# Kernel optimization log

Measured on AMD Instinct MI355X. Metric: run time of the kernel, lower is better.

Reference implementation:

```python
import jax, jax.numpy as jnp
import numpy as np

TOP_K = 2


def setup_inputs() -> dict:
    key = jax.random.key(0)
    k1, k2, k3, k4, k5 = jax.random.split(key, 5)
    T, H, I, E = 1024, 1024, 2816, 8
    return {
        "hidden_states": jax.random.normal(k1, (T, H), dtype=jnp.float32),
        "router_logits": jax.random.normal(k2, (T, E), dtype=jnp.float32),
        "w1": jax.random.normal(k3, (E, I, H), dtype=jnp.float32) * 0.02,
        "w3": jax.random.normal(k4, (E, I, H), dtype=jnp.float32) * 0.02,
        "w2": jax.random.normal(k5, (E, H, I), dtype=jnp.float32) * 0.02,
    }


def _gate_weights(router_logits):
    # top-k softmax with renormalization (Mixtral-style routing)
    probs = jax.nn.softmax(router_logits, axis=-1)          # [T, E]
    vals, idx = jax.lax.top_k(probs, TOP_K)                  # [T, K]
    vals = vals / jnp.sum(vals, axis=-1, keepdims=True)
    E = router_logits.shape[-1]
    # dense per-expert gate [T, E]: scatter top-k weights via one-hot
    onehot = jax.nn.one_hot(idx, E, dtype=vals.dtype)        # [T, K, E]
    return jnp.einsum("tk,tke->te", vals, onehot)


def reference(hidden_states, router_logits, w1, w3, w2):
    x = hidden_states.reshape(-1, hidden_states.shape[-1])   # [T, H]
    gate = _gate_weights(router_logits)                      # [T, E]
    # GatedMLP per expert: silu(x @ w1^T) * (x @ w3^T) @ w2^T
    h1 = jnp.einsum("th,eih->tei", x, w1)                    # [T, E, I]
    h3 = jnp.einsum("th,eih->tei", x, w3)
    act = jax.nn.silu(h1) * h3                               # [T, E, I]
    y = jnp.einsum("tei,ehi->teh", act, w2)                  # [T, E, H]
    out = jnp.einsum("teh,te->th", y, gate)                  # weighted combine
    return out
```

## Files before the change

### kernel.cpp

```cpp
#include <hip/hip_runtime.h>
#include <stdint.h>

#define T_TOK 1024
#define H_DIM 1024
#define I_DIM 2816
#define E_NUM 8
#define KSPLIT 4
#define K2_STEPS (I_DIM / 64 / KSPLIT)

typedef __attribute__((ext_vector_type(8))) short bf16x8;
typedef __attribute__((ext_vector_type(4))) float f32x4;

struct Meta { int counts[E_NUM]; int tiles[E_NUM]; int offs[E_NUM]; };

__device__ __forceinline__ unsigned short f2b(float f) {
    unsigned u = __float_as_uint(f);
    u += 0x7fffu + ((u >> 16) & 1u);
    return (unsigned short)(u >> 16);
}

__device__ __forceinline__ uint4 pack8(const float4 a, const float4 b) {
    union { unsigned short us[8]; uint4 v; } u;
    u.us[0] = f2b(a.x); u.us[1] = f2b(a.y); u.us[2] = f2b(a.z); u.us[3] = f2b(a.w);
    u.us[4] = f2b(b.x); u.us[5] = f2b(b.y); u.us[6] = f2b(b.z); u.us[7] = f2b(b.w);
    return u.v;
}

__global__ void route_kernel(const float* __restrict__ logits,
                             int* __restrict__ tok, float* __restrict__ gate,
                             Meta* __restrict__ meta) {
    __shared__ int cnt[E_NUM];
    const int tid = threadIdx.x;
    if (tid < E_NUM) cnt[tid] = 0;
    for (int j = tid; j < E_NUM * T_TOK; j += 1024) { tok[j] = 0; gate[j] = 0.f; }
    __syncthreads();

    float p[E_NUM];
    const float* lrow = logits + tid * E_NUM;
    float m = -1e30f;
    #pragma unroll
    for (int e = 0; e < E_NUM; ++e) { p[e] = lrow[e]; m = fmaxf(m, p[e]); }
    #pragma unroll
    for (int e = 0; e < E_NUM; ++e) p[e] = __expf(p[e] - m);
    int e0 = 0; float v0 = p[0];
    #pragma unroll
    for (int e = 1; e < E_NUM; ++e) if (p[e] > v0) { v0 = p[e]; e0 = e; }
    int e1 = -1; float v1 = -1.f;
    #pragma unroll
    for (int e = 0; e < E_NUM; ++e) if (e != e0 && p[e] > v1) { v1 = p[e]; e1 = e; }
    const float inv = 1.f / (v0 + v1);
    const float g0 = v0 * inv, g1 = v1 * inv;

    const int p0 = atomicAdd(&cnt[e0], 1);
    const int p1 = atomicAdd(&cnt[e1], 1);
    tok[e0 * T_TOK + p0] = tid; gate[e0 * T_TOK + p0] = g0;
    tok[e1 * T_TOK + p1] = tid; gate[e1 * T_TOK + p1] = g1;
    __syncthreads();
    if (tid == 0) {
        int off = 0;
        for (int e = 0; e < E_NUM; ++e) {
            const int c = cnt[e];
            const int t = (c + 127) >> 7;
            meta->counts[e] = c; meta->tiles[e] = t; meta->offs[e] = off;
            off += t * 128;
        }
    }
}

__global__ void cvt_x_kernel(const float* __restrict__ x, unsigned short* __restrict__ xb) {
    const int i = blockIdx.x * blockDim.x + threadIdx.x;
    const float4 v = ((const float4*)x)[i];
    ushort4 o; o.x = f2b(v.x); o.y = f2b(v.y); o.z = f2b(v.z); o.w = f2b(v.w);
    ((ushort4*)xb)[i] = o;
}

__launch_bounds__(512)
__global__ void gemm1_kernel(const unsigned short* __restrict__ xb,
                             const float* __restrict__ w1,
                             const float* __restrict__ w3,
                             const int* __restrict__ tok,
                             const Meta* __restrict__ meta,
                             unsigned short* __restrict__ act) {
    const int e = blockIdx.y;
    const int mt = blockIdx.z;
    if (mt >= meta->tiles[e]) return;
    const int it = blockIdx.x;
    const int tid = threadIdx.x;

    __shared__ __align__(16) unsigned short As[128 * 64];
    __shared__ __align__(16) unsigned short B1s[64 * 64];
    __shared__ __align__(16) unsigned short B3s[64 * 64];

    const int srow = tid >> 3, ssub = tid & 7;
    const int t0 = tok[e * T_TOK + mt * 128 + srow];
    const int t1 = tok[e * T_TOK + mt * 128 + 64 + srow];
    const unsigned short* ap0 = xb + (size_t)t0 * H_DIM + ssub * 8;
    const unsigned short* ap1 = xb + (size_t)t1 * H_DIM + ssub * 8;
    const int scol = (ssub * 8) ^ ((srow & 7) << 3);
    unsigned short* al0 = &As[srow * 64 + scol];
    unsigned short* al1 = &As[(64 + srow) * 64 + scol];

    const size_t wbase = (size_t)e * I_DIM * H_DIM + (size_t)(it * 64 + srow) * H_DIM + ssub * 8;
    const float* b1p = w1 + wbase;
    const float* b3p = w3 + wbase;
    unsigned short* bl1 = &B1s[srow * 64 + scol];
    unsigned short* bl3 = &B3s[srow * 64 + scol];

    const int wave = tid >> 6, lane = tid & 63;
    const int quad = lane >> 4, l15 = lane & 15;
    const int mbase = (wave >> 1) * 32;
    const int nbase = (wave & 1) * 32;

    f32x4 acc1[2][2], acc3[2][2];
    #pragma unroll
    for (int m = 0; m < 2; ++m)
        #pragma unroll
        for (int n = 0; n < 2; ++n) {
            acc1[m][n] = (f32x4){0.f, 0.f, 0.f, 0.f};
            acc3[m][n] = (f32x4){0.f, 0.f, 0.f, 0.f};
        }

    uint4 ra0 = *(const uint4*)ap0, ra1 = *(const uint4*)ap1;
    float4 rb1a = *(const float4*)b1p, rb1b = *(const float4*)(b1p + 4);
    float4 rb3a = *(const float4*)b3p, rb3b = *(const float4*)(b3p + 4);

    const int NK = H_DIM / 64;
    for (int ks = 0; ks < NK; ++ks) {
        __syncthreads();
        *(uint4*)al0 = ra0;
        *(uint4*)al1 = ra1;
        *(uint4*)bl1 = pack8(rb1a, rb1b);
        *(uint4*)bl3 = pack8(rb3a, rb3b);
        __syncthreads();
        if (ks + 1 < NK) {
            const int k0 = (ks + 1) * 64;
            ra0 = *(const uint4*)(ap0 + k0);  ra1 = *(const uint4*)(ap1 + k0);
            rb1a = *(const float4*)(b1p + k0); rb1b = *(const float4*)(b1p + k0 + 4);
            rb3a = *(const float4*)(b3p + k0); rb3b = *(const float4*)(b3p + k0 + 4);
        }
        bf16x8 a[2][2], bf1[2][2], bf3[2][2];
        #pragma unroll
        for (int m = 0; m < 2; ++m) {
            const int row = mbase + m * 16 + l15;
            #pragma unroll
            for (int kk = 0; kk < 2; ++kk)
                a[m][kk] = *(const bf16x8*)&As[row * 64 + ((kk * 32 + quad * 8) ^ ((row & 7) << 3))];
        }
        #pragma unroll
        for (int n = 0; n < 2; ++n) {
            const int row = nbase + n * 16 + l15;
            #pragma unroll
            for (int kk = 0; kk < 2; ++kk) {
                const int off = row * 64 + ((kk * 32 + quad * 8) ^ ((row & 7) << 3));
                bf1[n][kk] = *(const bf16x8*)&B1s[off];
                bf3[n][kk] = *(const bf16x8*)&B3s[off];
            }
        }
        #pragma unroll
        for (int m = 0; m < 2; ++m)
            #pragma unroll
            for (int n = 0; n < 2; ++n)
                #pragma unroll
                for (int kk = 0; kk < 2; ++kk) {
                    acc1[m][n] = __builtin_amdgcn_mfma_f32_16x16x32_bf16(a[m][kk], bf1[n][kk], acc1[m][n], 0, 0, 0);
                    acc3[m][n] = __builtin_amdgcn_mfma_f32_16x16x32_bf16(a[m][kk], bf3[n][kk], acc3[m][n], 0, 0, 0);
                }
    }

    const int opad = meta->offs[e];
    #pragma unroll
    for (int m = 0; m < 2; ++m)
        #pragma unroll
        for (int n = 0; n < 2; ++n)
            #pragma unroll
            for (int rr = 0; rr < 4; ++rr) {
                const float v1 = acc1[m][n][rr];
                const float v3 = acc3[m][n][rr];
                const float s = v1 / (1.f + __expf(-v1)) * v3;
                const int row = opad + mt * 128 + mbase + m * 16 + quad * 4 + rr;
                const int col = it * 64 + nbase + n * 16 + l15;
                act[(size_t)row * I_DIM + col] = f2b(s);
            }
}

__launch_bounds__(512)
__global__ void gemm2_kernel(const unsigned short* __restrict__ act,
                             const float* __restrict__ w2,
                             const int* __restrict__ tok,
                             const float* __restrict__ gate,
                             const Meta* __restrict__ meta,
                             float* __restrict__ out) {
    const int e = blockIdx.y;
    const int mt = blockIdx.z >> 2;
    const int kb = blockIdx.z & 3;
    if (mt >= meta->tiles[e]) return;
    const int it = blockIdx.x;
    const int tid = threadIdx.x;
    const int opad = meta->offs[e];

    __shared__ __align__(16) unsigned short As[128 * 64];
    __shared__ __align__(16) unsigned short Bs[64 * 64];

    const int srow = tid >> 3, ssub = tid & 7;
    const int kbase = kb * (K2_STEPS * 64);
    const unsigned short* ap0 = act + (size_t)(opad + mt * 128 + srow) * I_DIM + kbase + ssub * 8;
    const unsigned short* ap1 = ap0 + (size_t)64 * I_DIM;
    const int scol = (ssub * 8) ^ ((srow & 7) << 3);
    unsigned short* al0 = &As[srow * 64 + scol];
    unsigned short* al1 = &As[(64 + srow) * 64 + scol];

    const float* bp = w2 + (size_t)e * H_DIM * I_DIM + (size_t)(it * 64 + srow) * I_DIM + kbase + ssub * 8;
    unsigned short* bl = &Bs[srow * 64 + scol];

    const int wave = tid >> 6, lane = tid & 63;
    const int quad = lane >> 4, l15 = lane & 15;
    const int mbase = (wave >> 1) * 32;
    const int nbase = (wave & 1) * 32;

    f32x4 acc[2][2];
    #pragma unroll
    for (int m = 0; m < 2; ++m)
        #pragma unroll
        for (int n = 0; n < 2; ++n) acc[m][n] = (f32x4){0.f, 0.f, 0.f, 0.f};

    uint4 ra0 = *(const uint4*)ap0, ra1 = *(const uint4*)ap1;
    float4 rba = *(const float4*)bp, rbb = *(const float4*)(bp + 4);

    for (int ks = 0; ks < K2_STEPS; ++ks) {
        __syncthreads();
        *(uint4*)al0 = ra0;
        *(uint4*)al1 = ra1;
        *(uint4*)bl = pack8(rba, rbb);
        __syncthreads();
        if (ks + 1 < K2_STEPS) {
            const int k0 = (ks + 1) * 64;
            ra0 = *(const uint4*)(ap0 + k0); ra1 = *(const uint4*)(ap1 + k0);
            rba = *(const float4*)(bp + k0); rbb = *(const float4*)(bp + k0 + 4);
        }
        bf16x8 a[2][2], bf[2][2];
        #pragma unroll
        for (int m = 0; m < 2; ++m) {
            const int row = mbase + m * 16 + l15;
            #pragma unroll
            for (int kk = 0; kk < 2; ++kk)
                a[m][kk] = *(const bf16x8*)&As[row * 64 + ((kk * 32 + quad * 8) ^ ((row & 7) << 3))];
        }
        #pragma unroll
        for (int n = 0; n < 2; ++n) {
            const int row = nbase + n * 16 + l15;
            #pragma unroll
            for (int kk = 0; kk < 2; ++kk)
                bf[n][kk] = *(const bf16x8*)&Bs[row * 64 + ((kk * 32 + quad * 8) ^ ((row & 7) << 3))];
        }
        #pragma unroll
        for (int m = 0; m < 2; ++m)
            #pragma unroll
            for (int n = 0; n < 2; ++n)
                #pragma unroll
                for (int kk = 0; kk < 2; ++kk)
                    acc[m][n] = __builtin_amdgcn_mfma_f32_16x16x32_bf16(a[m][kk], bf[n][kk], acc[m][n], 0, 0, 0);
    }

    #pragma unroll
    for (int m = 0; m < 2; ++m)
        #pragma unroll
        for (int rr = 0; rr < 4; ++rr) {
            const int r = mt * 128 + mbase + m * 16 + quad * 4 + rr;
            const int t = tok[e * T_TOK + r];
            const float g = gate[e * T_TOK + r];
            if (g != 0.f) {
                #pragma unroll
                for (int n = 0; n < 2; ++n) {
                    const int col = it * 64 + nbase + n * 16 + l15;
                    atomicAdd(&out[(size_t)t * H_DIM + col], g * acc[m][n][rr]);
                }
            }
        }
}

extern "C" void kernel_launch(void* const* d_in, const int* in_sizes, int n_in,
                              void* d_out, int out_size, void* d_ws, size_t ws_size,
                              hipStream_t stream) {
    const float* x      = (const float*)d_in[0];
    const float* logits = (const float*)d_in[1];
    const float* w1     = (const float*)d_in[2];
    const float* w3     = (const float*)d_in[3];
    const float* w2     = (const float*)d_in[4];
    float* out = (float*)d_out;

    char* ws = (char*)d_ws;
    int*   tok  = (int*)ws;
    float* gate = (float*)(ws + 32768);
    Meta*  meta = (Meta*)(ws + 65536);
    unsigned short* xb  = (unsigned short*)(ws + 131072);
    unsigned short* act = (unsigned short*)(ws + 131072 + 2097152);

    hipMemsetAsync(d_out, 0, (size_t)T_TOK * H_DIM * sizeof(float), stream);
    route_kernel<<<1, 1024, 0, stream>>>(logits, tok, gate, meta);
    cvt_x_kernel<<<T_TOK * H_DIM / 4 / 256, 256, 0, stream>>>(x, xb);
    gemm1_kernel<<<dim3(I_DIM / 64, E_NUM, 8), 512, 0, stream>>>(xb, w1, w3, tok, meta, act);
    gemm2_kernel<<<dim3(H_DIM / 64, E_NUM, 8 * KSPLIT), 512, 0, stream>>>(act, w2, tok, gate, meta, out);
}
```

Baseline: 339.2 us.

## Double-buffer GEMM LDS tiles and replace atomic scatter with deterministic combine kernel

Both expert GEMMs now use two LDS buffers with register prefetch two steps ahead, so each iteration needs one barrier instead of two. The second GEMM drops from four K-splits to two and writes partial sums to a workspace instead of atomically adding into the output. A new combine kernel applies the gate weights and sums the two expert rows per token, which also removes the output memset. The cost is an extra launch and extra workspace traffic, and the doubled LDS use with occupancy hints may affect register allocation.

```diff
diff --git a/kernel.cpp b/kernel.cpp
--- a/kernel.cpp
+++ b/kernel.cpp
@@ -5,8 +5,9 @@
 #define H_DIM 1024
 #define I_DIM 2816
 #define E_NUM 8
-#define KSPLIT 4
+#define KSPLIT 2
 #define K2_STEPS (I_DIM / 64 / KSPLIT)
+#define MAXROWS 3072
 
 typedef __attribute__((ext_vector_type(8))) short bf16x8;
 typedef __attribute__((ext_vector_type(4))) float f32x4;
@@ -26,13 +27,17 @@
     return u.v;
 }
 
+#define SYNC_RAW() do { asm volatile("s_waitcnt lgkmcnt(0)" ::: "memory"); __builtin_amdgcn_s_barrier(); } while (0)
+
 __global__ void route_kernel(const float* __restrict__ logits,
-                             int* __restrict__ tok, float* __restrict__ gate,
+                             int* __restrict__ tok,
+                             int4* __restrict__ comb,
                              Meta* __restrict__ meta) {
     __shared__ int cnt[E_NUM];
+    __shared__ int soffs[E_NUM];
     const int tid = threadIdx.x;
     if (tid < E_NUM) cnt[tid] = 0;
-    for (int j = tid; j < E_NUM * T_TOK; j += 1024) { tok[j] = 0; gate[j] = 0.f; }
+    for (int j = tid; j < E_NUM * T_TOK; j += 1024) tok[j] = 0;
     __syncthreads();
 
     float p[E_NUM];
@@ -53,8 +58,8 @@
 
     const int p0 = atomicAdd(&cnt[e0], 1);
     const int p1 = atomicAdd(&cnt[e1], 1);
-    tok[e0 * T_TOK + p0] = tid; gate[e0 * T_TOK + p0] = g0;
-    tok[e1 * T_TOK + p1] = tid; gate[e1 * T_TOK + p1] = g1;
+    tok[e0 * T_TOK + p0] = tid;
+    tok[e1 * T_TOK + p1] = tid;
     __syncthreads();
     if (tid == 0) {
         int off = 0;
@@ -62,9 +67,13 @@
             const int c = cnt[e];
             const int t = (c + 127) >> 7;
             meta->counts[e] = c; meta->tiles[e] = t; meta->offs[e] = off;
+            soffs[e] = off;
             off += t * 128;
         }
     }
+    __syncthreads();
+    comb[tid] = make_int4(soffs[e0] + p0, soffs[e1] + p1,
+                          __float_as_int(g0), __float_as_int(g1));
 }
 
 __global__ void cvt_x_kernel(const float* __restrict__ x, unsigned short* __restrict__ xb) {
@@ -74,7 +83,7 @@
     ((ushort4*)xb)[i] = o;
 }
 
-__launch_bounds__(512)
+__launch_bounds__(512, 4)
 __global__ void gemm1_kernel(const unsigned short* __restrict__ xb,
                              const float* __restrict__ w1,
                              const float* __restrict__ w3,
@@ -87,9 +96,9 @@
     const int it = blockIdx.x;
     const int tid = threadIdx.x;
 
-    __shared__ __align__(16) unsigned short As[128 * 64];
-    __shared__ __align__(16) unsigned short B1s[64 * 64];
-    __shared__ __align__(16) unsigned short B3s[64 * 64];
+    __shared__ __align__(16) unsigned short As[2][128 * 64];
+    __shared__ __align__(16) unsigned short B1s[2][64 * 64];
+    __shared__ __align__(16) unsigned short B3s[2][64 * 64];
 
     const int srow = tid >> 3, ssub = tid & 7;
     const int t0 = tok[e * T_TOK + mt * 128 + srow];
@@ -97,14 +106,13 @@
     const unsigned short* ap0 = xb + (size_t)t0 * H_DIM + ssub * 8;
     const unsigned short* ap1 = xb + (size_t)t1 * H_DIM + ssub * 8;
     const int scol = (ssub * 8) ^ ((srow & 7) << 3);
-    unsigned short* al0 = &As[srow * 64 + scol];
-    unsigned short* al1 = &As[(64 + srow) * 64 + scol];
+    const int aoff0 = srow * 64 + scol;
+    const int aoff1 = (64 + srow) * 64 + scol;
+    const int boff  = srow * 64 + scol;
 
     const size_t wbase = (size_t)e * I_DIM * H_DIM + (size_t)(it * 64 + srow) * H_DIM + ssub * 8;
     const float* b1p = w1 + wbase;
     const float* b3p = w3 + wbase;
-    unsigned short* bl1 = &B1s[srow * 64 + scol];
-    unsigned short* bl3 = &B3s[srow * 64 + scol];
 
     const int wave = tid >> 6, lane = tid & 63;
     const int quad = lane >> 4, l15 = lane & 15;
@@ -120,52 +128,71 @@
             acc3[m][n] = (f32x4){0.f, 0.f, 0.f, 0.f};
         }
 
-    uint4 ra0 = *(const uint4*)ap0, ra1 = *(const uint4*)ap1;
-    float4 rb1a = *(const float4*)b1p, rb1b = *(const float4*)(b1p + 4);
-    float4 rb3a = *(const float4*)b3p, rb3b = *(const float4*)(b3p + 4);
+#define G1_LOAD(S, koff) do { \
+        S##_a0  = *(const uint4*)(ap0 + (koff));      S##_a1  = *(const uint4*)(ap1 + (koff)); \
+        S##_b1a = *(const float4*)(b1p + (koff));     S##_b1b = *(const float4*)(b1p + (koff) + 4); \
+        S##_b3a = *(const float4*)(b3p + (koff));     S##_b3b = *(const float4*)(b3p + (koff) + 4); \
+    } while (0)
+
+#define G1_STORE(S, B) do { \
+        *(uint4*)&As[B][aoff0] = S##_a0; \
+        *(uint4*)&As[B][aoff1] = S##_a1; \
+        *(uint4*)&B1s[B][boff] = pack8(S##_b1a, S##_b1b); \
+        *(uint4*)&B3s[B][boff] = pack8(S##_b3a, S##_b3b); \
+    } while (0)
+
+#define G1_COMPUTE(B) do { \
+        bf16x8 afr[2][2], f1[2][2], f3[2][2]; \
+        _Pragma("unroll") \
+        for (int m = 0; m < 2; ++m) { \
+            const int row = mbase + m * 16 + l15; \
+            _Pragma("unroll") \
+            for (int kk = 0; kk < 2; ++kk) \
+                afr[m][kk] = *(const bf16x8*)&As[B][row * 64 + ((kk * 32 + quad * 8) ^ ((row & 7) << 3))]; \
+        } \
+        _Pragma("unroll") \
+        for (int n = 0; n < 2; ++n) { \
+            const int row = nbase + n * 16 + l15; \
+            _Pragma("unroll") \
+            for (int kk = 0; kk < 2; ++kk) { \
+                const int off = row * 64 + ((kk * 32 + quad * 8) ^ ((row & 7) << 3)); \
+                f1[n][kk] = *(const bf16x8*)&B1s[B][off]; \
+                f3[n][kk] = *(const bf16x8*)&B3s[B][off]; \
+            } \
+        } \
+        _Pragma("unroll") \
+        for (int m = 0; m < 2; ++m) \
+            _Pragma("unroll") \
+            for (int n = 0; n < 2; ++n) \
+                _Pragma("unroll") \
+                for (int kk = 0; kk < 2; ++kk) { \
+                    acc1[m][n] = __builtin_amdgcn_mfma_f32_16x16x32_bf16(afr[m][kk], f1[n][kk], acc1[m][n], 0, 0, 0); \
+                    acc3[m][n] = __builtin_amdgcn_mfma_f32_16x16x32_bf16(afr[m][kk], f3[n][kk], acc3[m][n], 0, 0, 0); \
+                } \
+    } while (0)
+
+    uint4 s0_a0, s0_a1; float4 s0_b1a, s0_b1b, s0_b3a, s0_b3b;
+    uint4 s1_a0, s1_a1; float4 s1_b1a, s1_b1b, s1_b3a, s1_b3b;
 
     const int NK = H_DIM / 64;
-    for (int ks = 0; ks < NK; ++ks) {
-        __syncthreads();
-        *(uint4*)al0 = ra0;
-        *(uint4*)al1 = ra1;
-        *(uint4*)bl1 = pack8(rb1a, rb1b);
-        *(uint4*)bl3 = pack8(rb3a, rb3b);
-        __syncthreads();
-        if (ks + 1 < NK) {
-            const int k0 = (ks + 1) * 64;
-            ra0 = *(const uint4*)(ap0 + k0);  ra1 = *(const uint4*)(ap1 + k0);
-            rb1a = *(const float4*)(b1p + k0); rb1b = *(const float4*)(b1p + k0 + 4);
-            rb3a = *(const float4*)(b3p + k0); rb3b = *(const float4*)(b3p + k0 + 4);
-        }
-        bf16x8 a[2][2], bf1[2][2], bf3[2][2];
-        #pragma unroll
-        for (int m = 0; m < 2; ++m) {
-            const int row = mbase + m * 16 + l15;
-            #pragma unroll
-            for (int kk = 0; kk < 2; ++kk)
-                a[m][kk] = *(const bf16x8*)&As[row * 64 + ((kk * 32 + quad * 8) ^ ((row & 7) << 3))];
-        }
-        #pragma unroll
-        for (int n = 0; n < 2; ++n) {
-            const int row = nbase + n * 16 + l15;
-            #pragma unroll
-            for (int kk = 0; kk < 2; ++kk) {
-                const int off = row * 64 + ((kk * 32 + quad * 8) ^ ((row & 7) << 3));
-                bf1[n][kk] = *(const bf16x8*)&B1s[off];
-                bf3[n][kk] = *(const bf16x8*)&B3s[off];
-            }
-        }
-        #pragma unroll
-        for (int m = 0; m < 2; ++m)
-            #pragma unroll
-            for (int n = 0; n < 2; ++n)
-                #pragma unroll
-                for (int kk = 0; kk < 2; ++kk) {
-                    acc1[m][n] = __builtin_amdgcn_mfma_f32_16x16x32_bf16(a[m][kk], bf1[n][kk], acc1[m][n], 0, 0, 0);
-                    acc3[m][n] = __builtin_amdgcn_mfma_f32_16x16x32_bf16(a[m][kk], bf3[n][kk], acc3[m][n], 0, 0, 0);
-                }
+    G1_LOAD(s0, 0);
+    G1_STORE(s0, 0);
+    G1_LOAD(s1, 64);
+    SYNC_RAW();
+
+    for (int ks = 0; ks < NK; ks += 2) {
+        { const int k2 = (ks + 2 < NK) ? (ks + 2) * 64 : 0; G1_LOAD(s0, k2); }
+        G1_COMPUTE(0);
+        G1_STORE(s1, 1);
+        SYNC_RAW();
+        { const int k3 = (ks + 3 < NK) ? (ks + 3) * 64 : 0; G1_LOAD(s1, k3); }
+        G1_COMPUTE(1);
+        G1_STORE(s0, 0);
+        SYNC_RAW();
     }
+#undef G1_LOAD
+#undef G1_STORE
+#undef G1_COMPUTE
 
     const int opad = meta->offs[e];
     #pragma unroll
@@ -183,34 +210,32 @@
             }
 }
 
-__launch_bounds__(512)
+__launch_bounds__(512, 4)
 __global__ void gemm2_kernel(const unsigned short* __restrict__ act,
                              const float* __restrict__ w2,
-                             const int* __restrict__ tok,
-                             const float* __restrict__ gate,
                              const Meta* __restrict__ meta,
-                             float* __restrict__ out) {
+                             float* __restrict__ ybuf) {
     const int e = blockIdx.y;
-    const int mt = blockIdx.z >> 2;
-    const int kb = blockIdx.z & 3;
+    const int mt = blockIdx.z >> 1;
+    const int kb = blockIdx.z & 1;
     if (mt >= meta->tiles[e]) return;
     const int it = blockIdx.x;
     const int tid = threadIdx.x;
     const int opad = meta->offs[e];
 
-    __shared__ __align__(16) unsigned short As[128 * 64];
-    __shared__ __align__(16) unsigned short Bs[64 * 64];
+    __shared__ __align__(16) unsigned short As[2][128 * 64];
+    __shared__ __align__(16) unsigned short Bs[2][64 * 64];
 
     const int srow = tid >> 3, ssub = tid & 7;
     const int kbase = kb * (K2_STEPS * 64);
     const unsigned short* ap0 = act + (size_t)(opad + mt * 128 + srow) * I_DIM + kbase + ssub * 8;
     const unsigned short* ap1 = ap0 + (size_t)64 * I_DIM;
     const int scol = (ssub * 8) ^ ((srow & 7) << 3);
-    unsigned short* al0 = &As[srow * 64 + scol];
-    unsigned short* al1 = &As[(64 + srow) * 64 + scol];
+    const int aoff0 = srow * 64 + scol;
+    const int aoff1 = (64 + srow) * 64 + scol;
+    const int boff  = srow * 64 + scol;
 
     const float* bp = w2 + (size_t)e * H_DIM * I_DIM + (size_t)(it * 64 + srow) * I_DIM + kbase + ssub * 8;
-    unsigned short* bl = &Bs[srow * 64 + scol];
 
     const int wave = tid >> 6, lane = tid & 63;
     const int quad = lane >> 4, l15 = lane & 15;
@@ -223,59 +248,96 @@
         #pragma unroll
         for (int n = 0; n < 2; ++n) acc[m][n] = (f32x4){0.f, 0.f, 0.f, 0.f};
 
-    uint4 ra0 = *(const uint4*)ap0, ra1 = *(const uint4*)ap1;
-    float4 rba = *(const float4*)bp, rbb = *(const float4*)(bp + 4);
-
-    for (int ks = 0; ks < K2_STEPS; ++ks) {
-        __syncthreads();
-        *(uint4*)al0 = ra0;
-        *(uint4*)al1 = ra1;
-        *(uint4*)bl = pack8(rba, rbb);
-        __syncthreads();
-        if (ks + 1 < K2_STEPS) {
-            const int k0 = (ks + 1) * 64;
-            ra0 = *(const uint4*)(ap0 + k0); ra1 = *(const uint4*)(ap1 + k0);
-            rba = *(const float4*)(bp + k0); rbb = *(const float4*)(bp + k0 + 4);
-        }
-        bf16x8 a[2][2], bf[2][2];
-        #pragma unroll
-        for (int m = 0; m < 2; ++m) {
-            const int row = mbase + m * 16 + l15;
-            #pragma unroll
-            for (int kk = 0; kk < 2; ++kk)
-                a[m][kk] = *(const bf16x8*)&As[row * 64 + ((kk * 32 + quad * 8) ^ ((row & 7) << 3))];
-        }
-        #pragma unroll
-        for (int n = 0; n < 2; ++n) {
-            const int row = nbase + n * 16 + l15;
-            #pragma unroll
-            for (int kk = 0; kk < 2; ++kk)
-                bf[n][kk] = *(const bf16x8*)&Bs[row * 64 + ((kk * 32 + quad * 8) ^ ((row & 7) << 3))];
-        }
-        #pragma unroll
-        for (int m = 0; m < 2; ++m)
-            #pragma unroll
-            for (int n = 0; n < 2; ++n)
-                #pragma unroll
-                for (int kk = 0; kk < 2; ++kk)
-                    acc[m][n] = __builtin_amdgcn_mfma_f32_16x16x32_bf16(a[m][kk], bf[n][kk], acc[m][n], 0, 0, 0);
+#define G2_LOAD(S, koff) do { \
+        S##_a0 = *(const uint4*)(ap0 + (koff));  S##_a1 = *(const uint4*)(ap1 + (koff)); \
+        S##_ba = *(const float4*)(bp + (koff));  S##_bb = *(const float4*)(bp + (koff) + 4); \
+    } while (0)
+
+#define G2_STORE(S, B) do { \
+        *(uint4*)&As[B][aoff0] = S##_a0; \
+        *(uint4*)&As[B][aoff1] = S##_a1; \
+        *(uint4*)&Bs[B][boff]  = pack8(S##_ba, S##_bb); \
+    } while (0)
+
+#define G2_COMPUTE(B) do { \
+        bf16x8 afr[2][2], bfr[2][2]; \
+        _Pragma("unroll") \
+        for (int m = 0; m < 2; ++m) { \
+            const int row = mbase + m * 16 + l15; \
+            _Pragma("unroll") \
+            for (int kk = 0; kk < 2; ++kk) \
+                afr[m][kk] = *(const bf16x8*)&As[B][row * 64 + ((kk * 32 + quad * 8) ^ ((row & 7) << 3))]; \
+        } \
+        _Pragma("unroll") \
+        for (int n = 0; n < 2; ++n) { \
+            const int row = nbase + n * 16 + l15; \
+            _Pragma("unroll") \
+            for (int kk = 0; kk < 2; ++kk) \
+                bfr[n][kk] = *(const bf16x8*)&Bs[B][row * 64 + ((kk * 32 + quad * 8) ^ ((row & 7) << 3))]; \
+        } \
+        _Pragma("unroll") \
+        for (int m = 0; m < 2; ++m) \
+            _Pragma("unroll") \
+            for (int n = 0; n < 2; ++n) \
+                _Pragma("unroll") \
+                for (int kk = 0; kk < 2; ++kk) \
+                    acc[m][n] = __builtin_amdgcn_mfma_f32_16x16x32_bf16(afr[m][kk], bfr[n][kk], acc[m][n], 0, 0, 0); \
+    } while (0)
+
+    uint4 s0_a0, s0_a1; float4 s0_ba, s0_bb;
+    uint4 s1_a0, s1_a1; float4 s1_ba, s1_bb;
+
+    G2_LOAD(s0, 0);
+    G2_STORE(s0, 0);
+    G2_LOAD(s1, 64);
+    SYNC_RAW();
+
+    for (int ks = 0; ks < K2_STEPS; ks += 2) {
+        { const int k2 = (ks + 2 < K2_STEPS) ? (ks + 2) * 64 : 0; G2_LOAD(s0, k2); }
+        G2_COMPUTE(0);
+        G2_STORE(s1, 1);
+        SYNC_RAW();
+        { const int k3 = (ks + 3 < K2_STEPS) ? (ks + 3) * 64 : 0; G2_LOAD(s1, k3); }
+        G2_COMPUTE(1);
+        G2_STORE(s0, 0);
+        SYNC_RAW();
     }
-
+#undef G2_LOAD
+#undef G2_STORE
+#undef G2_COMPUTE
+
+    float* yb = ybuf + (size_t)kb * ((size_t)MAXROWS * H_DIM);
     #pragma unroll
     for (int m = 0; m < 2; ++m)
         #pragma unroll
         for (int rr = 0; rr < 4; ++rr) {
-            const int r = mt * 128 + mbase + m * 16 + quad * 4 + rr;
-            const int t = tok[e * T_TOK + r];
-            const float g = gate[e * T_TOK + r];
-            if (g != 0.f) {
-                #pragma unroll
-                for (int n = 0; n < 2; ++n) {
-                    const int col = it * 64 + nbase + n * 16 + l15;
-                    atomicAdd(&out[(size_t)t * H_DIM + col], g * acc[m][n][rr]);
-                }
+            const int grow = opad + mt * 128 + mbase + m * 16 + quad * 4 + rr;
+            #pragma unroll
+            for (int n = 0; n < 2; ++n) {
+                const int col = it * 64 + nbase + n * 16 + l15;
+                yb[(size_t)grow * H_DIM + col] = acc[m][n][rr];
             }
         }
+}
+
+__global__ void combine_kernel(const float* __restrict__ ybuf,
+                               const int4* __restrict__ comb,
+                               float* __restrict__ out) {
+    const int t = blockIdx.x;
+    const int c = threadIdx.x;
+    const int4 cb = comb[t];
+    const float g0 = __int_as_float(cb.z), g1 = __int_as_float(cb.w);
+    const size_t sp = (size_t)MAXROWS * H_DIM;
+    const float4 a = ((const float4*)(ybuf + (size_t)cb.x * H_DIM))[c];
+    const float4 b = ((const float4*)(ybuf + sp + (size_t)cb.x * H_DIM))[c];
+    const float4 d = ((const float4*)(ybuf + (size_t)cb.y * H_DIM))[c];
+    const float4 f = ((const float4*)(ybuf + sp + (size_t)cb.y * H_DIM))[c];
+    float4 o;
+    o.x = g0 * (a.x + b.x) + g1 * (d.x + f.x);
+    o.y = g0 * (a.y + b.y) + g1 * (d.y + f.y);
+    o.z = g0 * (a.z + b.z) + g1 * (d.z + f.z);
+    o.w = g0 * (a.w + b.w) + g1 * (d.w + f.w);
+    ((float4*)(out + (size_t)t * H_DIM))[c] = o;
 }
 
 extern "C" void kernel_launch(void* const* d_in, const int* in_sizes, int n_in,
@@ -290,14 +352,15 @@
 
     char* ws = (char*)d_ws;
     int*   tok  = (int*)ws;
-    float* gate = (float*)(ws + 32768);
     Meta*  meta = (Meta*)(ws + 65536);
+    int4*  comb = (int4*)(ws + 69632);
     unsigned short* xb  = (unsigned short*)(ws + 131072);
-    unsigned short* act = (unsigned short*)(ws + 131072 + 2097152);
-
-    hipMemsetAsync(d_out, 0, (size_t)T_TOK * H_DIM * sizeof(float), stream);
-    route_kernel<<<1, 1024, 0, stream>>>(logits, tok, gate, meta);
+    unsigned short* act = (unsigned short*)(ws + 2228224);
+    float* ybuf = (float*)(ws + 19529728);
+
+    route_kernel<<<1, 1024, 0, stream>>>(logits, tok, comb, meta);
     cvt_x_kernel<<<T_TOK * H_DIM / 4 / 256, 256, 0, stream>>>(x, xb);
     gemm1_kernel<<<dim3(I_DIM / 64, E_NUM, 8), 512, 0, stream>>>(xb, w1, w3, tok, meta, act);
-    gemm2_kernel<<<dim3(H_DIM / 64, E_NUM, 8 * KSPLIT), 512, 0, stream>>>(act, w2, tok, gate, meta, out);
-}
+    gemm2_kernel<<<dim3(H_DIM / 64, E_NUM, 8 * KSPLIT), 512, 0, stream>>>(act, w2, meta, ybuf);
+    combine_kernel<<<T_TOK, 256, 0, stream>>>(ybuf, comb, out);
+}
```

After: 332.5 us. 1.02x faster.

## Replace atomic scatter-add in down-projection with split-K buffers and combine kernel

Applied to the files above, without the earlier changes.

The down-projection GEMM now writes plain per-row partial results into two split-K buffers instead of atomically adding gated values into the output. A new combine kernel gathers each token's two expert rows from both K halves, applies the gates and writes the output directly, so the output memset is no longer needed. The router emits a per-token record of padded row positions and gates for this gather. The change removes atomic contention and the memset, at the cost of an extra launch and extra intermediate traffic of roughly 2x3072x1024 floats. Split-K drops from 4 to 2, which halves the number of gemm2 blocks.

```diff
diff --git a/kernel.cpp b/kernel.cpp
--- a/kernel.cpp
+++ b/kernel.cpp
@@ -5,8 +5,9 @@
 #define H_DIM 1024
 #define I_DIM 2816
 #define E_NUM 8
-#define KSPLIT 4
+#define KSPLIT 2
 #define K2_STEPS (I_DIM / 64 / KSPLIT)
+#define MAXROWS 3072
 
 typedef __attribute__((ext_vector_type(8))) short bf16x8;
 typedef __attribute__((ext_vector_type(4))) float f32x4;
@@ -27,12 +28,14 @@
 }
 
 __global__ void route_kernel(const float* __restrict__ logits,
-                             int* __restrict__ tok, float* __restrict__ gate,
+                             int* __restrict__ tok,
+                             int4* __restrict__ comb,
                              Meta* __restrict__ meta) {
     __shared__ int cnt[E_NUM];
+    __shared__ int soffs[E_NUM];
     const int tid = threadIdx.x;
     if (tid < E_NUM) cnt[tid] = 0;
-    for (int j = tid; j < E_NUM * T_TOK; j += 1024) { tok[j] = 0; gate[j] = 0.f; }
+    for (int j = tid; j < E_NUM * T_TOK; j += 1024) tok[j] = 0;
     __syncthreads();
 
     float p[E_NUM];
@@ -53,8 +56,8 @@
 
     const int p0 = atomicAdd(&cnt[e0], 1);
     const int p1 = atomicAdd(&cnt[e1], 1);
-    tok[e0 * T_TOK + p0] = tid; gate[e0 * T_TOK + p0] = g0;
-    tok[e1 * T_TOK + p1] = tid; gate[e1 * T_TOK + p1] = g1;
+    tok[e0 * T_TOK + p0] = tid;
+    tok[e1 * T_TOK + p1] = tid;
     __syncthreads();
     if (tid == 0) {
         int off = 0;
@@ -62,9 +65,13 @@
             const int c = cnt[e];
             const int t = (c + 127) >> 7;
             meta->counts[e] = c; meta->tiles[e] = t; meta->offs[e] = off;
+            soffs[e] = off;
             off += t * 128;
         }
     }
+    __syncthreads();
+    comb[tid] = make_int4(soffs[e0] + p0, soffs[e1] + p1,
+                          __float_as_int(g0), __float_as_int(g1));
 }
 
 __global__ void cvt_x_kernel(const float* __restrict__ x, unsigned short* __restrict__ xb) {
@@ -186,23 +193,21 @@
 __launch_bounds__(512)
 __global__ void gemm2_kernel(const unsigned short* __restrict__ act,
                              const float* __restrict__ w2,
-                             const int* __restrict__ tok,
-                             const float* __restrict__ gate,
                              const Meta* __restrict__ meta,
-                             float* __restrict__ out) {
+                             float* __restrict__ ybuf) {
     const int e = blockIdx.y;
-    const int mt = blockIdx.z >> 2;
-    const int kb = blockIdx.z & 3;
+    const int mt = blockIdx.z >> 1;
+    const int kb = blockIdx.z & 1;
     if (mt >= meta->tiles[e]) return;
     const int it = blockIdx.x;
     const int tid = threadIdx.x;
     const int opad = meta->offs[e];
+    const int kbase = kb * (K2_STEPS * 64);
 
     __shared__ __align__(16) unsigned short As[128 * 64];
     __shared__ __align__(16) unsigned short Bs[64 * 64];
 
     const int srow = tid >> 3, ssub = tid & 7;
-    const int kbase = kb * (K2_STEPS * 64);
     const unsigned short* ap0 = act + (size_t)(opad + mt * 128 + srow) * I_DIM + kbase + ssub * 8;
     const unsigned short* ap1 = ap0 + (size_t)64 * I_DIM;
     const int scol = (ssub * 8) ^ ((srow & 7) << 3);
@@ -261,21 +266,38 @@
                     acc[m][n] = __builtin_amdgcn_mfma_f32_16x16x32_bf16(a[m][kk], bf[n][kk], acc[m][n], 0, 0, 0);
     }
 
+    float* yb = ybuf + (size_t)kb * ((size_t)MAXROWS * H_DIM);
     #pragma unroll
     for (int m = 0; m < 2; ++m)
         #pragma unroll
         for (int rr = 0; rr < 4; ++rr) {
-            const int r = mt * 128 + mbase + m * 16 + quad * 4 + rr;
-            const int t = tok[e * T_TOK + r];
-            const float g = gate[e * T_TOK + r];
-            if (g != 0.f) {
-                #pragma unroll
-                for (int n = 0; n < 2; ++n) {
-                    const int col = it * 64 + nbase + n * 16 + l15;
-                    atomicAdd(&out[(size_t)t * H_DIM + col], g * acc[m][n][rr]);
-                }
+            const int grow = opad + mt * 128 + mbase + m * 16 + quad * 4 + rr;
+            #pragma unroll
+            for (int n = 0; n < 2; ++n) {
+                const int col = it * 64 + nbase + n * 16 + l15;
+                yb[(size_t)grow * H_DIM + col] = acc[m][n][rr];
             }
         }
+}
+
+__global__ void combine_kernel(const float* __restrict__ ybuf,
+                               const int4* __restrict__ comb,
+                               float* __restrict__ out) {
+    const int t = blockIdx.x;
+    const int c = threadIdx.x;
+    const int4 cb = comb[t];
+    const float g0 = __int_as_float(cb.z), g1 = __int_as_float(cb.w);
+    const size_t sp = (size_t)MAXROWS * H_DIM;
+    const float4 a = ((const float4*)(ybuf + (size_t)cb.x * H_DIM))[c];
+    const float4 b = ((const float4*)(ybuf + sp + (size_t)cb.x * H_DIM))[c];
+    const float4 d = ((const float4*)(ybuf + (size_t)cb.y * H_DIM))[c];
+    const float4 f = ((const float4*)(ybuf + sp + (size_t)cb.y * H_DIM))[c];
+    float4 o;
+    o.x = g0 * (a.x + b.x) + g1 * (d.x + f.x);
+    o.y = g0 * (a.y + b.y) + g1 * (d.y + f.y);
+    o.z = g0 * (a.z + b.z) + g1 * (d.z + f.z);
+    o.w = g0 * (a.w + b.w) + g1 * (d.w + f.w);
+    ((float4*)(out + (size_t)t * H_DIM))[c] = o;
 }
 
 extern "C" void kernel_launch(void* const* d_in, const int* in_sizes, int n_in,
@@ -290,14 +312,15 @@
 
     char* ws = (char*)d_ws;
     int*   tok  = (int*)ws;
-    float* gate = (float*)(ws + 32768);
     Meta*  meta = (Meta*)(ws + 65536);
+    int4*  comb = (int4*)(ws + 69632);
     unsigned short* xb  = (unsigned short*)(ws + 131072);
-    unsigned short* act = (unsigned short*)(ws + 131072 + 2097152);
-
-    hipMemsetAsync(d_out, 0, (size_t)T_TOK * H_DIM * sizeof(float), stream);
-    route_kernel<<<1, 1024, 0, stream>>>(logits, tok, gate, meta);
+    unsigned short* act = (unsigned short*)(ws + 2228224);
+    float* ybuf = (float*)(ws + 19529728);
+
+    route_kernel<<<1, 1024, 0, stream>>>(logits, tok, comb, meta);
     cvt_x_kernel<<<T_TOK * H_DIM / 4 / 256, 256, 0, stream>>>(x, xb);
     gemm1_kernel<<<dim3(I_DIM / 64, E_NUM, 8), 512, 0, stream>>>(xb, w1, w3, tok, meta, act);
-    gemm2_kernel<<<dim3(H_DIM / 64, E_NUM, 8 * KSPLIT), 512, 0, stream>>>(act, w2, tok, gate, meta, out);
-}
+    gemm2_kernel<<<dim3(H_DIM / 64, E_NUM, 8 * KSPLIT), 512, 0, stream>>>(act, w2, meta, ybuf);
+    combine_kernel<<<T_TOK, 256, 0, stream>>>(ybuf, comb, out);
+}
```

After: 323.7 us. -4.6%, faster.
